# Performance work log

Measured on AMD Instinct MI355X. Metric: run time of the kernel, lower is better.

The kernel has to match this reference:

```python
import jax, jax.numpy as jnp
import numpy as np

NUM_HEADS = 16
EMBED_DIM = 2048
HEAD_DIM = EMBED_DIM // NUM_HEADS


def setup_inputs() -> dict:
    key = jax.random.key(0)
    ks = jax.random.split(key, 11)
    B, SQ, SKV = 4, 512, 3584
    x = jax.random.normal(ks[0], (B, SQ, EMBED_DIM), dtype=jnp.float32)
    v = jax.random.normal(ks[1], (B, SKV, NUM_HEADS, HEAD_DIM), dtype=jnp.float32)
    k = jax.random.normal(ks[2], (B, SKV, NUM_HEADS, HEAD_DIM), dtype=jnp.float32)
    s = 0.02
    Wv = jax.random.normal(ks[3], (EMBED_DIM, EMBED_DIM), dtype=jnp.float32) * s
    bv = jnp.zeros((EMBED_DIM,), dtype=jnp.float32)
    Wq = jax.random.normal(ks[4], (EMBED_DIM, EMBED_DIM), dtype=jnp.float32) * s
    bq = jnp.zeros((EMBED_DIM,), dtype=jnp.float32)
    Wk = jax.random.normal(ks[5], (EMBED_DIM, EMBED_DIM), dtype=jnp.float32) * s
    bk = jnp.zeros((EMBED_DIM,), dtype=jnp.float32)
    Wo = jax.random.normal(ks[6], (EMBED_DIM, EMBED_DIM), dtype=jnp.float32) * s
    bo = jnp.zeros((EMBED_DIM,), dtype=jnp.float32)
    return {"x": x, "v": v, "k": k, "Wv": Wv, "bv": bv, "Wq": Wq, "bq": bq,
            "Wk": Wk, "bk": bk, "Wo": Wo, "bo": bo}


def reference(x, v, k, Wv, bv, Wq, bq, Wk, bk, Wo, bo):
    B, SQ, E = x.shape
    # QKV projections (flax Dense: y = x @ kernel + bias), split into heads
    v_i = (x @ Wv + bv).reshape(B, SQ, NUM_HEADS, HEAD_DIM)
    q_i = (x @ Wq + bq).reshape(B, SQ, NUM_HEADS, HEAD_DIM)
    k_i = (x @ Wk + bk).reshape(B, SQ, NUM_HEADS, HEAD_DIM)
    # Append new keys/values to the cache
    v_new = jnp.concatenate((v, v_i), axis=1)  # [B, Skv+Sq, H, Dh]
    k_new = jnp.concatenate((k, k_i), axis=1)
    # Scaled dot-product attention over the full (extended) cache
    scale = 1.0 / jnp.sqrt(jnp.asarray(HEAD_DIM, dtype=x.dtype))
    attn = jnp.einsum('bqhd,bkhd->bhqk', q_i, k_new) * scale  # [B,H,Sq,Skv+Sq]
    attn = jax.nn.softmax(attn, axis=-1)
    values = jnp.einsum('bhqk,bkhd->bqhd', attn, v_new).reshape(B, SQ, E)
    out_i = values @ Wo + bo
    return (v_new, k_new, out_i)
```

## Files before the change

kernel.cpp:

```cpp
#include <hip/hip_runtime.h>
#include <hip/hip_bf16.h>
#include <stdint.h>

typedef float  f32x4 __attribute__((ext_vector_type(4)));
typedef short  s16x8 __attribute__((ext_vector_type(8)));
typedef unsigned short u16;

#define E_DIM 2048
#define NHEAD 16
#define DHEAD 128
#define NB    4
#define SQL   512
#define STOT  4096
#define SKV   3584
#define KOFF  ((size_t)33554432)
#define OOFF  ((size_t)67108864)

static __device__ __forceinline__ u16 f2b(float f){
  union { float f; uint32_t u; } v; v.f = f;
  uint32_t u = v.u;
  uint32_t r = ((u >> 16) & 1u) + 0x7fffu;
  return (u16)((u + r) >> 16);
}

static __device__ __forceinline__ float redmax16(float v){
  v = fmaxf(v, __shfl_xor(v, 1));
  v = fmaxf(v, __shfl_xor(v, 2));
  v = fmaxf(v, __shfl_xor(v, 4));
  v = fmaxf(v, __shfl_xor(v, 8));
  return v;
}
static __device__ __forceinline__ float redsum16(float v){
  v += __shfl_xor(v, 1);
  v += __shfl_xor(v, 2);
  v += __shfl_xor(v, 4);
  v += __shfl_xor(v, 8);
  return v;
}

#define GLD_LDS16(gp, lp) \
  __builtin_amdgcn_global_load_lds((const __attribute__((address_space(1))) void*)(gp), \
                                   (__attribute__((address_space(3))) void*)(lp), 16, 0, 0)

#define SWZV(d) ((((d) ^ ((d) >> 3)) & 7) << 4)

__global__ __launch_bounds__(256) void prep_kernel(
    const float* __restrict__ x, u16* __restrict__ xbf,
    const float* __restrict__ Wq, const float* __restrict__ Wk,
    const float* __restrict__ Wv, const float* __restrict__ Wo,
    u16* __restrict__ wt)
{
  __shared__ float tile[64][65];
  const int bid = blockIdx.x;
  const int t = threadIdx.x;
  if (bid >= 4096){
    size_t i = (size_t)(bid - 4096) * 256 + t;
    f32x4 a = __builtin_nontemporal_load((const f32x4*)x + 2*i);
    f32x4 b = __builtin_nontemporal_load((const f32x4*)x + 2*i + 1);
    union { u16 us[8]; uint4 v; } r;
    r.us[0]=f2b(a[0]); r.us[1]=f2b(a[1]); r.us[2]=f2b(a[2]); r.us[3]=f2b(a[3]);
    r.us[4]=f2b(b[0]); r.us[5]=f2b(b[1]); r.us[6]=f2b(b[2]); r.us[7]=f2b(b[3]);
    ((uint4*)xbf)[i] = r.v;
    return;
  }
  const int z = bid >> 10, rem = bid & 1023;
  const float* src = (z==0)?Wq : (z==1)?Wk : (z==2)?Wv : Wo;
  u16* dst = wt + (size_t)z * E_DIM * E_DIM;
  const int r0 = (rem & 31)*64, c0 = (rem >> 5)*64;
  #pragma unroll 4
  for (int it=0; it<16; it++){
    int idx = it*256 + t; int r = idx>>6, c = idx&63;
    tile[r][c] = __builtin_nontemporal_load(src + (size_t)(r0+r)*E_DIM + c0 + c);
  }
  __syncthreads();
  #pragma unroll 4
  for (int it=0; it<16; it++){
    int idx = it*256 + t; int rr = idx>>6, cc = idx&63;
    dst[(size_t)(c0+rr)*E_DIM + r0 + cc] = f2b(tile[cc][rr]);
  }
}

__global__ __launch_bounds__(256) void qkvcopy_kernel(
    const u16* __restrict__ A, const u16* __restrict__ Wt,
    const float* __restrict__ b0, const float* __restrict__ b1, const float* __restrict__ b2,
    const float* __restrict__ vsrc, const float* __restrict__ ksrc,
    float* __restrict__ dout, u16* __restrict__ qbf,
    u16* __restrict__ kcb, u16* __restrict__ vcb, int usebf)
{
  __shared__ __align__(16) u16 As[128*32];
  __shared__ __align__(16) u16 Bs[128*32];
  const int bid = blockIdx.x;
  const int t = threadIdx.x;

  if (bid >= 768){
    int cid = bid - 768;
    int arr = (cid >= 7168);
    int c2 = arr ? cid - 7168 : cid;
    int b = c2 / 1792;
    int xb = c2 - b*1792;
    const f32x4* s4 = (const f32x4*)((arr ? ksrc : vsrc) + (size_t)b*7340032);
    f32x4* d4       = (f32x4*)(dout + (arr ? KOFF : 0) + (size_t)b*8388608);
    u16*   db       = (arr ? kcb : vcb) + (size_t)b*8388608;
    #pragma unroll
    for (int it=0; it<4; it++){
      int idx = xb*1024 + it*256 + t;
      f32x4 val = __builtin_nontemporal_load(s4 + idx);
      __builtin_nontemporal_store(val, d4 + idx);
      if (usebf){
        union { u16 us[4]; uint2 u; } p;
        p.us[0]=f2b(val[0]); p.us[1]=f2b(val[1]); p.us[2]=f2b(val[2]); p.us[3]=f2b(val[3]);
        *(uint2*)(db + (size_t)idx*4) = p.u;
      }
    }
    return;
  }

  const int l = t & 63, w = t >> 6;
  const int lr = l & 15, lh = l >> 4;
  const int m0 = (bid & 15) * 128;
  const int y  = bid >> 4;
  const int mat = y >> 4;
  const int n0  = (y & 15) * 128;
  const u16* Bp = Wt + (size_t)mat * E_DIM * E_DIM;
  const float* bias = (mat==0 ? b0 : (mat==1 ? b1 : b2));
  const int wm = (w>>1)*64, wn = (w&1)*64;

  f32x4 acc[4][4] = {};

  for (int k0 = 0; k0 < E_DIM; k0 += 32){
    __syncthreads();
    #pragma unroll
    for (int it=0; it<2; it++){
      int c = it*256 + t;
      int row = c>>2, j = c&3, g = j ^ (row&3);
      GLD_LDS16(Bp + (size_t)(n0+row)*E_DIM + k0 + g*8, (char*)Bs + c*16);
      GLD_LDS16(A  + (size_t)(m0+row)*E_DIM + k0 + g*8, (char*)As + c*16);
    }
    __syncthreads();
    s16x8 af[4], bfr[4];
    #pragma unroll
    for (int m=0;m<4;m++){
      int row = wm + m*16 + lr;
      af[m] = *(const s16x8*)((const char*)As + row*64 + ((lh ^ (row&3))<<4));
    }
    #pragma unroll
    for (int n=0;n<4;n++){
      int nn = wn + n*16 + lr;
      bfr[n] = *(const s16x8*)((const char*)Bs + nn*64 + ((lh ^ (nn&3))<<4));
    }
    __builtin_amdgcn_s_setprio(1);
    #pragma unroll
    for (int m=0;m<4;m++)
      #pragma unroll
      for (int n=0;n<4;n++)
        acc[m][n] = __builtin_amdgcn_mfma_f32_16x16x32_bf16(af[m], bfr[n], acc[m][n], 0,0,0);
    __builtin_amdgcn_s_setprio(0);
  }

  #pragma unroll
  for (int n=0;n<4;n++){
    int col = n0 + wn + n*16 + lr;
    float bc = bias[col];
    #pragma unroll
    for (int m=0;m<4;m++){
      int rbase = m0 + wm + m*16 + lh*4;
      #pragma unroll
      for (int j=0;j<4;j++){
        float val = acc[m][n][j] + bc;
        int row = rbase + j;
        if (mat == 0){
          qbf[(size_t)row*E_DIM + col] = f2b(val);
        } else {
          int b = row >> 9, sq = row & 511;
          size_t o = ((size_t)b*STOT + SKV + sq)*(size_t)E_DIM + col;
          float* ob = dout + (mat==1 ? KOFF : 0);
          __builtin_nontemporal_store(val, ob + o);
          if (usebf) (mat==1 ? kcb : vcb)[o] = f2b(val);
        }
      }
    }
  }
}

__global__ __launch_bounds__(256) void gemm_out_kernel(
    const u16* __restrict__ A, const u16* __restrict__ Wt,
    const float* __restrict__ bias, float* __restrict__ dout)
{
  __shared__ __align__(16) u16 As[64*32];
  __shared__ __align__(16) u16 Bs[128*32];
  const int t = threadIdx.x;
  const int l = t & 63, w = t >> 6;
  const int lr = l & 15, lh = l >> 4;
  const int m0 = blockIdx.x * 64;
  const int n0 = blockIdx.y * 128;
  const int wm = (w>>1)*32, wn = (w&1)*64;

  f32x4 acc[2][4] = {};

  for (int k0 = 0; k0 < E_DIM; k0 += 32){
    __syncthreads();
    #pragma unroll
    for (int it=0; it<2; it++){
      int c = it*256 + t;
      int row = c>>2, j = c&3, g = j ^ (row&3);
      GLD_LDS16(Wt + (size_t)(n0+row)*E_DIM + k0 + g*8, (char*)Bs + c*16);
      if (it==0)
        GLD_LDS16(A + (size_t)(m0+row)*E_DIM + k0 + g*8, (char*)As + c*16);
    }
    __syncthreads();
    s16x8 af[2], bfr[4];
    #pragma unroll
    for (int m=0;m<2;m++){
      int row = wm + m*16 + lr;
      af[m] = *(const s16x8*)((const char*)As + row*64 + ((lh ^ (row&3))<<4));
    }
    #pragma unroll
    for (int n=0;n<4;n++){
      int nn = wn + n*16 + lr;
      bfr[n] = *(const s16x8*)((const char*)Bs + nn*64 + ((lh ^ (nn&3))<<4));
    }
    __builtin_amdgcn_s_setprio(1);
    #pragma unroll
    for (int m=0;m<2;m++)
      #pragma unroll
      for (int n=0;n<4;n++)
        acc[m][n] = __builtin_amdgcn_mfma_f32_16x16x32_bf16(af[m], bfr[n], acc[m][n], 0,0,0);
    __builtin_amdgcn_s_setprio(0);
  }

  #pragma unroll
  for (int n=0;n<4;n++){
    int col = n0 + wn + n*16 + lr;
    float bc = bias[col];
    #pragma unroll
    for (int m=0;m<2;m++){
      int rbase = m0 + wm + m*16 + lh*4;
      #pragma unroll
      for (int j=0;j<4;j++){
        float val = acc[m][n][j] + bc;
        int row = rbase + j;
        __builtin_nontemporal_store(val, dout + OOFF + (size_t)row*E_DIM + col);
      }
    }
  }
}

template<int BF16KV>
__global__ __launch_bounds__(512) void attn_kernel(
    const u16* __restrict__ qbf,
    const u16* __restrict__ kcb, const u16* __restrict__ vcb,
    const float* __restrict__ kf32, const float* __restrict__ vf32,
    u16* __restrict__ valbf)
{
  __shared__ __align__(16) u16 Kt[2][64*128];
  __shared__ __align__(16) u16 Vt[2][128*64];
  __shared__ __align__(16) u16 Pl[8][16*64];
  const int t = threadIdx.x, l = t & 63, w = t >> 6;
  const int lr = l & 15, lh = l >> 4;
  const int n = blockIdx.x;
  const int o = (n & 7)*32 + (n >> 3);
  const int b = o >> 6, h = (o >> 2) & 15, qt = o & 3;
  const int qrow0 = qt*128 + w*16;

  const int sv_k4 = (t >> 5) * 4;
  const int sv_d0 = (t & 31) * 4;
  uint2 vreg[4];
  f32x4 vregf[4], kregf[4];

#define STAGE_ISSUE(S0N, NBUF) do {                                             \
    if (BF16KV){                                                                \
      _Pragma("unroll")                                                         \
      for (int it_=0; it_<2; it_++){                                            \
        int idx_ = it_*512 + t;                                                 \
        int key_ = idx_ >> 4, p_ = idx_ & 15, g_ = p_ ^ (key_ & 7);             \
        GLD_LDS16(kcb + ((size_t)b*STOT + (S0N) + key_)*E_DIM + h*DHEAD + g_*8, \
                  (char*)Kt[NBUF] + idx_*16);                                   \
      }                                                                         \
      _Pragma("unroll")                                                         \
      for (int i_=0; i_<4; i_++)                                                \
        vreg[i_] = *(const uint2*)(vcb + ((size_t)b*STOT + (S0N) + sv_k4 + i_)*E_DIM + h*DHEAD + sv_d0); \
    } else {                                                                    \
      _Pragma("unroll")                                                         \
      for (int it_=0; it_<2; it_++){                                            \
        int idx_ = it_*512 + t;                                                 \
        int key_ = idx_ >> 4, d0_ = (idx_ & 15)*8;                              \
        size_t src_ = ((size_t)b*STOT + (S0N) + key_)*E_DIM + h*DHEAD + d0_;    \
        kregf[2*it_]   = *(const f32x4*)(kf32 + src_);                          \
        kregf[2*it_+1] = *(const f32x4*)(kf32 + src_ + 4);                      \
      }                                                                         \
      _Pragma("unroll")                                                         \
      for (int i_=0; i_<4; i_++)                                                \
        vregf[i_] = *(const f32x4*)(vf32 + ((size_t)b*STOT + (S0N) + sv_k4 + i_)*E_DIM + h*DHEAD + sv_d0); \
    }                                                                           \
  } while(0)

#define STAGE_WRITE(NBUF) do {                                                  \
    u16 vv_[4][4];                                                              \
    if (BF16KV){                                                                \
      _Pragma("unroll")                                                         \
      for (int i_=0; i_<4; i_++){                                               \
        union { u16 us[4]; uint2 u; } r_; r_.u = vreg[i_];                      \
        vv_[i_][0]=r_.us[0]; vv_[i_][1]=r_.us[1]; vv_[i_][2]=r_.us[2]; vv_[i_][3]=r_.us[3]; \
      }                                                                         \
    } else {                                                                    \
      _Pragma("unroll")                                                         \
      for (int it_=0; it_<2; it_++){                                            \
        int idx_ = it_*512 + t;                                                 \
        int key_ = idx_ >> 4, d0_ = (idx_ & 15)*8;                              \
        union { u16 us[8]; s16x8 v; } p_;                                       \
        f32x4 f0_ = kregf[2*it_], f1_ = kregf[2*it_+1];                         \
        p_.us[0]=f2b(f0_[0]); p_.us[1]=f2b(f0_[1]); p_.us[2]=f2b(f0_[2]); p_.us[3]=f2b(f0_[3]); \
        p_.us[4]=f2b(f1_[0]); p_.us[5]=f2b(f1_[1]); p_.us[6]=f2b(f1_[2]); p_.us[7]=f2b(f1_[3]); \
        *(s16x8*)((char*)Kt[NBUF] + key_*256 + ((d0_*2) ^ ((key_&7)<<4))) = p_.v; \
      }                                                                         \
      _Pragma("unroll")                                                         \
      for (int i_=0; i_<4; i_++){                                               \
        vv_[i_][0]=f2b(vregf[i_][0]); vv_[i_][1]=f2b(vregf[i_][1]);             \
        vv_[i_][2]=f2b(vregf[i_][2]); vv_[i_][3]=f2b(vregf[i_][3]);             \
      }                                                                         \
    }                                                                           \
    _Pragma("unroll")                                                           \
    for (int dj_=0; dj_<4; dj_++){                                              \
      union { u16 us[4]; uint2 u; } p_;                                         \
      p_.us[0]=vv_[0][dj_]; p_.us[1]=vv_[1][dj_]; p_.us[2]=vv_[2][dj_]; p_.us[3]=vv_[3][dj_]; \
      int d_ = sv_d0 + dj_;                                                     \
      *(uint2*)((char*)Vt[NBUF] + d_*128 + ((sv_k4*2) ^ SWZV(d_))) = p_.u;      \
    }                                                                           \
  } while(0)

  s16x8 qf[4];
  #pragma unroll
  for (int kc=0; kc<4; kc++){
    int R = b*SQL + qrow0 + lr;
    int col = h*DHEAD + kc*32 + lh*8;
    qf[kc] = *(const s16x8*)(qbf + (size_t)R*E_DIM + col);
  }

  f32x4 accO[8] = {};
  float m_run[4], l_run[4];
  #pragma unroll
  for (int j=0; j<4; j++){ m_run[j] = -1e30f; l_run[j] = 0.f; }

  const float C = 0.08838834764831845f * 1.44269504088896f;

  STAGE_ISSUE(0, 0);
  STAGE_WRITE(0);
  __syncthreads();

  int cur = 0;
  for (int tt=0; tt<64; tt++){
    const int s0 = tt*64;
    const int nxt = cur ^ 1;
    if (tt < 63) STAGE_ISSUE(s0 + 64, nxt);

    f32x4 sv[4] = {};
    __builtin_amdgcn_s_setprio(1);
    #pragma unroll
    for (int kf=0; kf<4; kf++){
      int key = kf*16 + lr;
      #pragma unroll
      for (int kc=0; kc<4; kc++){
        s16x8 kb = *(const s16x8*)((char*)Kt[cur] + key*256 + ((kc*64 + lh*16) ^ ((key&7)<<4)));
        sv[kf] = __builtin_amdgcn_mfma_f32_16x16x32_bf16(qf[kc], kb, sv[kf], 0,0,0);
      }
    }
    __builtin_amdgcn_s_setprio(0);

    float vmj[4];
    float need = -1e30f;
    #pragma unroll
    for (int j=0; j<4; j++){
      float vm = fmaxf(fmaxf(sv[0][j], sv[1][j]), fmaxf(sv[2][j], sv[3][j]));
      vm = redmax16(vm);
      vmj[j] = vm;
      need = fmaxf(need, vm - m_run[j]);
    }
    const int skip = __all(need * C <= 8.0f);
    float alpha[4];
    #pragma unroll
    for (int j=0; j<4; j++){
      float mn = skip ? m_run[j] : fmaxf(m_run[j], vmj[j]);
      float a  = skip ? 1.0f : exp2f((m_run[j] - mn) * C);
      float rs = 0.f;
      #pragma unroll
      for (int kf=0; kf<4; kf++){
        float p = exp2f((sv[kf][j] - mn) * C);
        sv[kf][j] = p;
        rs += p;
      }
      rs = redsum16(rs);
      l_run[j] = l_run[j]*a + rs;
      m_run[j] = mn;
      alpha[j] = a;
    }
    if (!skip){
      #pragma unroll
      for (int nf=0; nf<8; nf++)
        #pragma unroll
        for (int j=0; j<4; j++)
          accO[nf][j] *= alpha[j];
    }
    #pragma unroll
    for (int kf=0; kf<4; kf++)
      #pragma unroll
      for (int j=0; j<4; j++){
        int row = lh*4 + j;
        int col = kf*16 + lr;
        *(u16*)((char*)Pl[w] + row*128 + ((col*2) ^ ((row&7)<<4))) = f2b(sv[kf][j]);
      }
    asm volatile("s_waitcnt lgkmcnt(0)" ::: "memory");
    __builtin_amdgcn_sched_barrier(0);

    #pragma unroll
    for (int kt=0; kt<2; kt++){
      s16x8 pa = *(const s16x8*)((char*)Pl[w] + lr*128 + ((kt*64 + lh*16) ^ ((lr&7)<<4)));
      __builtin_amdgcn_s_setprio(1);
      #pragma unroll
      for (int nf=0; nf<8; nf++){
        int d = nf*16 + lr;
        s16x8 vb = *(const s16x8*)((char*)Vt[cur] + d*128 + ((kt*64 + lh*16) ^ SWZV(d)));
        accO[nf] = __builtin_amdgcn_mfma_f32_16x16x32_bf16(pa, vb, accO[nf], 0,0,0);
      }
      __builtin_amdgcn_s_setprio(0);
    }

    if (tt < 63) STAGE_WRITE(nxt);
    __syncthreads();
    cur = nxt;
  }

  #pragma unroll
  for (int j=0; j<4; j++){
    float inv = 1.0f / l_run[j];
    int R = b*SQL + qrow0 + lh*4 + j;
    #pragma unroll
    for (int nf=0; nf<8; nf++){
      int col = h*DHEAD + nf*16 + lr;
      valbf[(size_t)R*E_DIM + col] = f2b(accO[nf][j] * inv);
    }
  }
#undef STAGE_ISSUE
#undef STAGE_WRITE
}

extern "C" void kernel_launch(void* const* d_in, const int* in_sizes, int n_in,
                              void* d_out, int out_size, void* d_ws, size_t ws_size,
                              hipStream_t stream){
  const float* x  = (const float*)d_in[0];
  const float* vc = (const float*)d_in[1];
  const float* kc = (const float*)d_in[2];
  const float* Wv = (const float*)d_in[3];
  const float* bv = (const float*)d_in[4];
  const float* Wq = (const float*)d_in[5];
  const float* bq = (const float*)d_in[6];
  const float* Wk = (const float*)d_in[7];
  const float* bk = (const float*)d_in[8];
  const float* Wo = (const float*)d_in[9];
  const float* bo = (const float*)d_in[10];
  float* out = (float*)d_out;
  char*  ws  = (char*)d_ws;

  u16* xbf  = (u16*)(ws);
  u16* wt   = (u16*)(ws + ((size_t)8  << 20));
  u16* qbf  = (u16*)(ws + ((size_t)40 << 20));
  u16* valb = (u16*)(ws + ((size_t)48 << 20));
  u16* kcb  = (u16*)(ws + ((size_t)56 << 20));
  u16* vcb  = (u16*)(ws + ((size_t)120 << 20));
  int usebf = (ws_size >= ((size_t)184 << 20)) ? 1 : 0;

  prep_kernel<<<6144, 256, 0, stream>>>(x, xbf, Wq, Wk, Wv, Wo, wt);
  qkvcopy_kernel<<<15104, 256, 0, stream>>>(xbf, wt, bq, bk, bv, vc, kc,
                                            out, qbf, kcb, vcb, usebf);
  if (usebf)
    attn_kernel<1><<<256, 512, 0, stream>>>(qbf, kcb, vcb, out + KOFF, out, valb);
  else
    attn_kernel<0><<<256, 512, 0, stream>>>(qbf, kcb, vcb, out + KOFF, out, valb);
  gemm_out_kernel<<<dim3(32,16), 256, 0, stream>>>(valb, wt + (size_t)3*E_DIM*E_DIM, bo, out);
}
```

Before: 788.9 us.

## Split attention KV range in two and merge partial softmax results

Attention now runs as a split-KV (flash-decoding style) pass. Each block covers half of the 4096 keys, so the grid grows from 256 to 512 blocks, which better fills the GPU's compute units. Each block writes an unnormalized bf16 partial output plus its running max and sum, and a new merge kernel combines the two halves with rescaling. The weight buffers are reshuffled so Wo sits in slot 0 and the partials can reuse freed workspace. The cost is an extra launch, extra global traffic for the partials, and a second bf16 rounding of the unnormalized outputs.

```diff
diff --git a/kernel.cpp b/kernel.cpp
--- a/kernel.cpp
+++ b/kernel.cpp
@@ -15,12 +15,16 @@
 #define SKV   3584
 #define KOFF  ((size_t)33554432)
 #define OOFF  ((size_t)67108864)
+#define CLOG  (0.08838834764831845f * 1.44269504088896f)
 
 static __device__ __forceinline__ u16 f2b(float f){
   union { float f; uint32_t u; } v; v.f = f;
   uint32_t u = v.u;
   uint32_t r = ((u >> 16) & 1u) + 0x7fffu;
   return (u16)((u + r) >> 16);
+}
+static __device__ __forceinline__ float b2f(u16 h){
+  union { uint32_t u; float f; } v; v.u = ((uint32_t)h) << 16; return v.f;
 }
 
 static __device__ __forceinline__ float redmax16(float v){
@@ -65,7 +69,8 @@
   }
   const int z = bid >> 10, rem = bid & 1023;
   const float* src = (z==0)?Wq : (z==1)?Wk : (z==2)?Wv : Wo;
-  u16* dst = wt + (size_t)z * E_DIM * E_DIM;
+  const int slot = (z + 1) & 3;
+  u16* dst = wt + (size_t)slot * E_DIM * E_DIM;
   const int r0 = (rem & 31)*64, c0 = (rem >> 5)*64;
   #pragma unroll 4
   for (int it=0; it<16; it++){
@@ -121,7 +126,7 @@
   const int y  = bid >> 4;
   const int mat = y >> 4;
   const int n0  = (y & 15) * 128;
-  const u16* Bp = Wt + (size_t)mat * E_DIM * E_DIM;
+  const u16* Bp = Wt + (size_t)(mat + 1) * E_DIM * E_DIM;
   const float* bias = (mat==0 ? b0 : (mat==1 ? b1 : b2));
   const int wm = (w>>1)*64, wn = (w&1)*64;
 
@@ -246,11 +251,11 @@
 }
 
 template<int BF16KV>
-__global__ __launch_bounds__(512) void attn_kernel(
+__global__ __launch_bounds__(512, 4) void attn_kernel(
     const u16* __restrict__ qbf,
     const u16* __restrict__ kcb, const u16* __restrict__ vcb,
     const float* __restrict__ kf32, const float* __restrict__ vf32,
-    u16* __restrict__ valbf)
+    u16* __restrict__ opart, float* __restrict__ mlp)
 {
   __shared__ __align__(16) u16 Kt[2][64*128];
   __shared__ __align__(16) u16 Vt[2][128*64];
@@ -258,9 +263,11 @@
   const int t = threadIdx.x, l = t & 63, w = t >> 6;
   const int lr = l & 15, lh = l >> 4;
   const int n = blockIdx.x;
-  const int o = (n & 7)*32 + (n >> 3);
-  const int b = o >> 6, h = (o >> 2) & 15, qt = o & 3;
+  const int o = (n & 7)*64 + (n >> 3);
+  const int bh = o >> 3, s = (o >> 2) & 1, qt = o & 3;
+  const int b = bh >> 4, h = bh & 15;
   const int qrow0 = qt*128 + w*16;
+  const int kvbase = s * 2048;
 
   const int sv_k4 = (t >> 5) * 4;
   const int sv_d0 = (t & 31) * 4;
@@ -341,17 +348,15 @@
   #pragma unroll
   for (int j=0; j<4; j++){ m_run[j] = -1e30f; l_run[j] = 0.f; }
 
-  const float C = 0.08838834764831845f * 1.44269504088896f;
-
-  STAGE_ISSUE(0, 0);
+  STAGE_ISSUE(kvbase, 0);
   STAGE_WRITE(0);
   __syncthreads();
 
   int cur = 0;
-  for (int tt=0; tt<64; tt++){
-    const int s0 = tt*64;
+  for (int tt=0; tt<32; tt++){
+    const int s0 = kvbase + tt*64;
     const int nxt = cur ^ 1;
-    if (tt < 63) STAGE_ISSUE(s0 + 64, nxt);
+    if (tt < 31) STAGE_ISSUE(s0 + 64, nxt);
 
     f32x4 sv[4] = {};
     __builtin_amdgcn_s_setprio(1);
@@ -375,16 +380,16 @@
       vmj[j] = vm;
       need = fmaxf(need, vm - m_run[j]);
     }
-    const int skip = __all(need * C <= 8.0f);
+    const int skip = __all(need * CLOG <= 8.0f);
     float alpha[4];
     #pragma unroll
     for (int j=0; j<4; j++){
       float mn = skip ? m_run[j] : fmaxf(m_run[j], vmj[j]);
-      float a  = skip ? 1.0f : exp2f((m_run[j] - mn) * C);
+      float a  = skip ? 1.0f : exp2f((m_run[j] - mn) * CLOG);
       float rs = 0.f;
       #pragma unroll
       for (int kf=0; kf<4; kf++){
-        float p = exp2f((sv[kf][j] - mn) * C);
+        float p = exp2f((sv[kf][j] - mn) * CLOG);
         sv[kf][j] = p;
         rs += p;
       }
@@ -424,23 +429,56 @@
       __builtin_amdgcn_s_setprio(0);
     }
 
-    if (tt < 63) STAGE_WRITE(nxt);
+    if (tt < 31) STAGE_WRITE(nxt);
     __syncthreads();
     cur = nxt;
   }
 
+  const size_t tilei = (size_t)(s*256 + bh*4 + qt);
+  const size_t obase = tilei * 16384;
   #pragma unroll
   for (int j=0; j<4; j++){
-    float inv = 1.0f / l_run[j];
-    int R = b*SQL + qrow0 + lh*4 + j;
-    #pragma unroll
-    for (int nf=0; nf<8; nf++){
-      int col = h*DHEAD + nf*16 + lr;
-      valbf[(size_t)R*E_DIM + col] = f2b(accO[nf][j] * inv);
-    }
+    int qlocal = w*16 + lh*4 + j;
+    if (lr == 0){
+      size_t mi = (tilei*128 + qlocal)*2;
+      mlp[mi]   = m_run[j];
+      mlp[mi+1] = l_run[j];
+    }
+    #pragma unroll
+    for (int nf=0; nf<8; nf++)
+      opart[obase + (size_t)qlocal*128 + nf*16 + lr] = f2b(accO[nf][j]);
   }
 #undef STAGE_ISSUE
 #undef STAGE_WRITE
+}
+
+__global__ __launch_bounds__(256) void merge_kernel(
+    const u16* __restrict__ opart, const float* __restrict__ mlp,
+    u16* __restrict__ valbf)
+{
+  const int t = threadIdx.x;
+  const int row = blockIdx.x*16 + (t >> 4);
+  const int d8  = (t & 15) * 8;
+  const int qlocal = row & 127, qt = (row >> 7) & 3, bh = row >> 9;
+  const int b = bh >> 4, h = bh & 15;
+  const size_t tile = (size_t)(bh*4 + qt);
+  const size_t po0 = (tile*128 + qlocal)*128 + d8;
+  const size_t po1 = po0 + (size_t)256*16384;
+  const size_t mi0 = (tile*128 + qlocal)*2;
+  const size_t mi1 = mi0 + (size_t)256*128*2;
+  const float m0 = mlp[mi0], l0 = mlp[mi0+1];
+  const float m1 = mlp[mi1], l1 = mlp[mi1+1];
+  const float m  = fmaxf(m0, m1);
+  const float w0 = exp2f((m0 - m) * CLOG);
+  const float w1 = exp2f((m1 - m) * CLOG);
+  const float invL = 1.0f / (l0*w0 + l1*w1);
+  union { u16 us[8]; uint4 v; } a, c, r;
+  a.v = *(const uint4*)(opart + po0);
+  c.v = *(const uint4*)(opart + po1);
+  #pragma unroll
+  for (int e=0; e<8; e++)
+    r.us[e] = f2b((b2f(a.us[e])*w0 + b2f(c.us[e])*w1) * invL);
+  *(uint4*)(valbf + ((size_t)(b*SQL + qt*128 + qlocal))*E_DIM + h*DHEAD + d8) = r.v;
 }
 
 extern "C" void kernel_launch(void* const* d_in, const int* in_sizes, int n_in,
@@ -460,20 +498,23 @@
   float* out = (float*)d_out;
   char*  ws  = (char*)d_ws;
 
-  u16* xbf  = (u16*)(ws);
-  u16* wt   = (u16*)(ws + ((size_t)8  << 20));
-  u16* qbf  = (u16*)(ws + ((size_t)40 << 20));
-  u16* valb = (u16*)(ws + ((size_t)48 << 20));
-  u16* kcb  = (u16*)(ws + ((size_t)56 << 20));
-  u16* vcb  = (u16*)(ws + ((size_t)120 << 20));
+  u16* xbf   = (u16*)(ws);
+  u16* wt    = (u16*)(ws + ((size_t)8  << 20));
+  u16* qbf   = (u16*)(ws + ((size_t)40 << 20));
+  u16* valb  = (u16*)(ws + ((size_t)48 << 20));
+  u16* kcb   = (u16*)(ws + ((size_t)56 << 20));
+  u16* vcb   = (u16*)(ws + ((size_t)120 << 20));
+  u16*   opart = (u16*)(ws + ((size_t)16 << 20));
+  float* mlp   = (float*)(ws + ((size_t)32 << 20));
   int usebf = (ws_size >= ((size_t)184 << 20)) ? 1 : 0;
 
   prep_kernel<<<6144, 256, 0, stream>>>(x, xbf, Wq, Wk, Wv, Wo, wt);
   qkvcopy_kernel<<<15104, 256, 0, stream>>>(xbf, wt, bq, bk, bv, vc, kc,
                                             out, qbf, kcb, vcb, usebf);
   if (usebf)
-    attn_kernel<1><<<256, 512, 0, stream>>>(qbf, kcb, vcb, out + KOFF, out, valb);
+    attn_kernel<1><<<512, 512, 0, stream>>>(qbf, kcb, vcb, out + KOFF, out, opart, mlp);
   else
-    attn_kernel<0><<<256, 512, 0, stream>>>(qbf, kcb, vcb, out + KOFF, out, valb);
-  gemm_out_kernel<<<dim3(32,16), 256, 0, stream>>>(valb, wt + (size_t)3*E_DIM*E_DIM, bo, out);
-}
+    attn_kernel<0><<<512, 512, 0, stream>>>(qbf, kcb, vcb, out + KOFF, out, opart, mlp);
+  merge_kernel<<<2048, 256, 0, stream>>>(opart, mlp, valb);
+  gemm_out_kernel<<<dim3(32,16), 256, 0, stream>>>(valb, wt, bo, out);
+}
```

Measured after the change: 1.030 ms. +30.6%, slower.
